# Kernel optimization log

Measured on AMD Instinct MI355X. Metric: run time of the kernel, lower is better.

Reference implementation:

```python
import jax, jax.numpy as jnp
import numpy as np

DIM = 512
H = 8
HS = DIM // H
SCALES = [25, 12, 7]
ATTN_SCALE = HS ** -0.5
EPS = 1e-5


def _ln(x, g, b):
    m = jnp.mean(x, axis=-1, keepdims=True)
    v = jnp.mean((x - m) ** 2, axis=-1, keepdims=True)
    return (x - m) * jax.lax.rsqrt(v + EPS) * g + b


def setup_inputs() -> dict:
    key = jax.random.key(0)
    ks = jax.random.split(key, 12)
    B, T, J, C = 64, 64, 25, DIM
    w = lambda k, s: jax.random.normal(k, s, dtype=jnp.float32) * 0.02
    return {
        "src": jax.random.normal(ks[0], (B, T, J, C), dtype=jnp.float32),
        "spatial_relation": jax.random.normal(ks[1], (B, T, J, J, 2), dtype=jnp.float32),
        "ln1_g": jnp.ones((C,), jnp.float32),
        "ln1_b": jnp.zeros((C,), jnp.float32),
        "Wq": w(ks[2], (3, C, C)),
        "Wk": w(ks[3], (3, C, C)),
        "Wv": w(ks[4], (3, C, C)),
        "pool0_fc1_w": w(ks[5], (C, 2 * C)),
        "pool0_fc1_b": jnp.zeros((2 * C,), jnp.float32),
        "pool0_fc2_w": w(ks[6], (2 * C, SCALES[1])),
        "pool0_fc2_b": jnp.zeros((SCALES[1],), jnp.float32),
        "pool1_fc1_w": w(ks[7], (C, 2 * C)),
        "pool1_fc1_b": jnp.zeros((2 * C,), jnp.float32),
        "pool1_fc2_w": w(ks[8], (2 * C, SCALES[2])),
        "pool1_fc2_b": jnp.zeros((SCALES[2],), jnp.float32),
    }


def reference(src, spatial_relation, ln1_g, ln1_b, Wq, Wk, Wv,
              pool0_fc1_w, pool0_fc1_b, pool0_fc2_w, pool0_fc2_b,
              pool1_fc1_w, pool1_fc1_b, pool1_fc2_w, pool1_fc2_b):
    # NOTE: in the original torch module, the relation-bias terms (R_qk, R_conv,
    # attn_R_qurt) and spatial_relation_emb are computed but never added to the
    # attention logits, so they do not affect the output; faithful output math below.
    B, T, J, C = src.shape
    x = src.reshape(B * T, J, C)
    g_feat = x  # global (query) features, stay at J nodes
    l_feat = x  # local (key/value) features, get pooled
    pools = [
        (pool0_fc1_w, pool0_fc1_b, pool0_fc2_w, pool0_fc2_b),
        (pool1_fc1_w, pool1_fc1_b, pool1_fc2_w, pool1_fc2_b),
    ]
    outs = []
    for i in range(len(SCALES)):
        qn = _ln(g_feat, ln1_g, ln1_b)
        kn = _ln(l_feat, ln1_g, ln1_b)
        q = (qn @ Wq[i]).reshape(B * T, J, H, HS)
        k = (kn @ Wk[i]).reshape(B * T, -1, H, HS)
        v = (kn @ Wv[i]).reshape(B * T, -1, H, HS)
        logits = jnp.einsum('bnhd,bmhd->bhnm', q, k) * ATTN_SCALE
        a = jax.nn.softmax(logits, axis=-1)
        o = jnp.einsum('bhnm,bmhd->bnhd', a, v).reshape(B * T, J, C)
        outs.append(g_feat + o)
        if i < len(SCALES) - 1:
            f1w, f1b, f2w, f2b = pools[i]
            h = jax.nn.gelu(l_feat @ f1w + f1b, approximate=False)
            S = jax.nn.softmax(h @ f2w + f2b, axis=-1)  # (BT, Ni, Ni+1)
            l_feat = jnp.einsum('bns,bnc->bsc', S, l_feat)
    return jnp.mean(jnp.stack(outs, axis=-1), axis=-1)
```

## Files before the change

### kernel.cpp

```cpp
#include <hip/hip_runtime.h>

typedef unsigned short u16;
typedef unsigned int   u32;
typedef _Float16 f16;
typedef __attribute__((ext_vector_type(8))) unsigned short u16x8;
typedef __attribute__((ext_vector_type(8))) _Float16 f16x8;
typedef __attribute__((ext_vector_type(2))) _Float16 f16x2;
typedef __attribute__((ext_vector_type(4))) float f32x4;

__device__ __forceinline__ u16 f2h(float f) {
  f16 h = (f16)f;
  return __builtin_bit_cast(u16, h);
}
__device__ __forceinline__ float h2f(u16 u) {
  return (float)__builtin_bit_cast(f16, u);
}

__global__ __launch_bounds__(256) void prep_w(const float* __restrict__ Wq,
    const float* __restrict__ Wk, const float* __restrict__ Wv,
    const float* __restrict__ f0, const float* __restrict__ f1,
    u16* __restrict__ wt) {
  int t = blockIdx.x * 256 + threadIdx.x;
  float v;
  if (t < 786432) {
    int i = t >> 18, r = t & 262143, n = r >> 9, k = r & 511;
    v = Wq[(size_t)(i << 18) + k * 512 + n];
  } else if (t < 2359296) {
    int r = t - 786432, i = r >> 19, r2 = r & 524287;
    int n = (r2 >> 9) & 511, k = r2 & 511;
    v = ((r2 >> 18) ? Wv : Wk)[(size_t)(i << 18) + k * 512 + n];
  } else if (t < 2883584) {
    int r = t - 2359296, n = r >> 9, k = r & 511;
    v = f0[(size_t)k * 1024 + n];
  } else {
    int r = t - 2883584, n = r >> 9, k = r & 511;
    v = f1[(size_t)k * 1024 + n];
  }
  wt[t] = f2h(v);
}

__global__ __launch_bounds__(256) void ln_f32(const float* __restrict__ x,
    const float* __restrict__ g, const float* __restrict__ bta,
    u16* __restrict__ xn, u16* __restrict__ xb) {
  int row = (blockIdx.x << 2) + (threadIdx.x >> 6);
  int lane = threadIdx.x & 63;
  const float* xr = x + (size_t)row * 512 + (lane << 3);
  float4 a = *(const float4*)xr;
  float4 c = *(const float4*)(xr + 4);
  float v[8] = {a.x, a.y, a.z, a.w, c.x, c.y, c.z, c.w};
  float s = 0.f, s2 = 0.f;
#pragma unroll
  for (int j = 0; j < 8; ++j) { s += v[j]; s2 += v[j] * v[j]; }
  for (int off = 32; off; off >>= 1) { s += __shfl_xor(s, off); s2 += __shfl_xor(s2, off); }
  float mean = s * (1.f / 512.f);
  float var = s2 * (1.f / 512.f) - mean * mean;
  float rs = rsqrtf(var + 1e-5f);
  const float* gp = g + (lane << 3);
  const float* bp = bta + (lane << 3);
  u16x8 pb, pn;
#pragma unroll
  for (int j = 0; j < 8; ++j) {
    pb[j] = f2h(v[j]);
    pn[j] = f2h((v[j] - mean) * rs * gp[j] + bp[j]);
  }
  *(u16x8*)(xb + (size_t)row * 512 + (lane << 3)) = pb;
  *(u16x8*)(xn + (size_t)row * 512 + (lane << 3)) = pn;
}

__global__ __launch_bounds__(256) void ln_b16(const u16* __restrict__ xin,
    const float* __restrict__ g, const float* __restrict__ bta,
    u16* __restrict__ xout) {
  int row = (blockIdx.x << 2) + (threadIdx.x >> 6);
  int lane = threadIdx.x & 63;
  f16x8 u = *(const f16x8*)(xin + (size_t)row * 512 + (lane << 3));
  float v[8];
#pragma unroll
  for (int j = 0; j < 8; ++j) v[j] = (float)u[j];
  float s = 0.f, s2 = 0.f;
#pragma unroll
  for (int j = 0; j < 8; ++j) { s += v[j]; s2 += v[j] * v[j]; }
  for (int off = 32; off; off >>= 1) { s += __shfl_xor(s, off); s2 += __shfl_xor(s2, off); }
  float mean = s * (1.f / 512.f);
  float var = s2 * (1.f / 512.f) - mean * mean;
  float rs = rsqrtf(var + 1e-5f);
  const float* gp = g + (lane << 3);
  const float* bp = bta + (lane << 3);
  u16x8 pn;
#pragma unroll
  for (int j = 0; j < 8; ++j) pn[j] = f2h((v[j] - mean) * rs * gp[j] + bp[j]);
  *(u16x8*)(xout + (size_t)row * 512 + (lane << 3)) = pn;
}

template <bool GELU>
__global__ __launch_bounds__(256, 2) void gemm_bt(const u16* __restrict__ A,
    const u16* __restrict__ Bt, u16* __restrict__ C,
    const float* __restrict__ bias, int M, int N) {
  __shared__ __align__(16) u16 As[128 * 64];
  __shared__ __align__(16) u16 Bs[128 * 64];
  int tid = threadIdx.x;
  int w = tid >> 6, lane = tid & 63;
  int nwg = gridDim.x * gridDim.y;
  int wg = blockIdx.x + gridDim.x * blockIdx.y;
  int swz = (wg & 7) * (nwg >> 3) + (wg >> 3);
  int m0 = (swz / gridDim.x) << 7, n0 = (swz % gridDim.x) << 7;
  int wm = (w & 1) << 6, wn = (w >> 1) << 6;
  f32x4 acc[4][4] = {};
  const int r_off = lane >> 3;
  const int k_off = (lane & 7) << 3;
  for (int kt = 0; kt < 8; ++kt) {
    __syncthreads();
#pragma unroll
    for (int j = 0; j < 4; ++j) {
      int q = (w << 2) + j;
      const u16* gA = A + (size_t)(m0 + (q << 3) + r_off) * 512 + (kt << 6) + k_off;
      __builtin_amdgcn_global_load_lds(
          (const __attribute__((address_space(1))) u32*)gA,
          (__attribute__((address_space(3))) u32*)(As + (q << 9)), 16, 0, 0);
      const u16* gB = Bt + (size_t)(n0 + (q << 3) + r_off) * 512 + (kt << 6) + k_off;
      __builtin_amdgcn_global_load_lds(
          (const __attribute__((address_space(1))) u32*)gB,
          (__attribute__((address_space(3))) u32*)(Bs + (q << 9)), 16, 0, 0);
    }
    asm volatile("s_waitcnt vmcnt(0)" ::: "memory");
    __syncthreads();
#pragma unroll
    for (int kk = 0; kk < 2; ++kk) {
      int ko = (kk << 5) + ((lane >> 4) << 3);
      f16x8 af[4], bfr[4];
#pragma unroll
      for (int mi = 0; mi < 4; ++mi)
        af[mi] = *(const f16x8*)(As + (wm + (mi << 4) + (lane & 15)) * 64 + ko);
#pragma unroll
      for (int ni = 0; ni < 4; ++ni)
        bfr[ni] = *(const f16x8*)(Bs + (wn + (ni << 4) + (lane & 15)) * 64 + ko);
#pragma unroll
      for (int mi = 0; mi < 4; ++mi)
#pragma unroll
        for (int ni = 0; ni < 4; ++ni)
          acc[mi][ni] = __builtin_amdgcn_mfma_f32_16x16x32_f16(af[mi], bfr[ni], acc[mi][ni], 0, 0, 0);
    }
  }
  int cr = (lane >> 4) << 2, cc = lane & 15;
#pragma unroll
  for (int mi = 0; mi < 4; ++mi) {
#pragma unroll
    for (int ni = 0; ni < 4; ++ni) {
      int col = n0 + wn + (ni << 4) + cc;
      float bv = 0.f;
      if (GELU) bv = bias[col];
#pragma unroll
      for (int j = 0; j < 4; ++j) {
        int row = m0 + wm + (mi << 4) + cr + j;
        float v = acc[mi][ni][j];
        if (GELU) { v += bv; v = 0.5f * v * (1.f + erff(v * 0.70710678118f)); }
        C[(size_t)row * N + col] = f2h(v);
      }
    }
  }
}

template <int NKV, int PMODE, int MINW>
__global__ __launch_bounds__(512, MINW) void attn(const u16* __restrict__ Q,
    const u16* __restrict__ KV, const u16* __restrict__ xb,
    float* __restrict__ out, u16* __restrict__ p) {
  constexpr int G = 8;
  constexpr int ELEMS = NKV * 1024;
  __shared__ __align__(16) u16 KVl[2][ELEMS];
  int tid = threadIdx.x;
  int b0 = blockIdx.x * G;
  int h = tid >> 6, r = tid & 63, n = r >> 1, half = r & 1;
  int dbase = (h << 6) + (half << 5);
  {
    const u16* src = KV + (size_t)b0 * ELEMS;
    for (int e = tid * 8; e < ELEMS; e += 4096)
      __builtin_amdgcn_global_load_lds(
          (const __attribute__((address_space(1))) u32*)(src + e),
          (__attribute__((address_space(3))) u32*)(KVl[0] + e), 16, 0, 0);
  }
  asm volatile("s_waitcnt vmcnt(0)" ::: "memory");
  __syncthreads();
  for (int t = 0; t < G; ++t) {
    const u16* KVc = KVl[t & 1];
    if (t + 1 < G) {
      const u16* src = KV + (size_t)(b0 + t + 1) * ELEMS;
      u16* dst = KVl[(t + 1) & 1];
      for (int e = tid * 8; e < ELEMS; e += 4096)
        __builtin_amdgcn_global_load_lds(
            (const __attribute__((address_space(1))) u32*)(src + e),
            (__attribute__((address_space(3))) u32*)(dst + e), 16, 0, 0);
    }
    int b = b0 + t;
    if (n < 25) {
      const u16* qr = Q + (size_t)(b * 25 + n) * 512 + dbase;
      f16x8 q8[4];
#pragma unroll
      for (int i = 0; i < 4; ++i) q8[i] = *(const f16x8*)(qr + (i << 3));
      const f16x2* q2 = (const f16x2*)q8;
      float s[NKV];
      float mx = -1e30f;
#pragma unroll
      for (int m = 0; m < NKV; ++m) {
        const u16* kr = KVc + m * 1024 + dbase;
        f16x2 a0 = {(f16)0.f, (f16)0.f}, a1 = a0;
#pragma unroll
        for (int i = 0; i < 4; ++i) {
          f16x8 kv = *(const f16x8*)(kr + (i << 3));
          const f16x2* k2 = (const f16x2*)&kv;
          a0 += q2[i * 4 + 0] * k2[0];
          a1 += q2[i * 4 + 1] * k2[1];
          a0 += q2[i * 4 + 2] * k2[2];
          a1 += q2[i * 4 + 3] * k2[3];
        }
        f16x2 at = a0 + a1;
        float d = (float)at[0] + (float)at[1];
        d += __shfl_xor(d, 1);
        s[m] = d * 0.125f;
        mx = fmaxf(mx, s[m]);
      }
      float sum = 0.f;
#pragma unroll
      for (int m = 0; m < NKV; ++m) { s[m] = __expf(s[m] - mx); sum += s[m]; }
      f16x8 o8[4] = {};
#pragma unroll
      for (int m = 0; m < NKV; ++m) {
        f16 ah = (f16)s[m];
        f16x8 av = {ah, ah, ah, ah, ah, ah, ah, ah};
        const u16* vr = KVc + m * 1024 + 512 + dbase;
#pragma unroll
        for (int i = 0; i < 4; ++i) {
          f16x8 vv = *(const f16x8*)(vr + (i << 3));
          o8[i] += vv * av;
        }
      }
      size_t rowoff = (size_t)(b * 25 + n) * 512 + dbase;
      if (PMODE == 0 || PMODE == 1) {
        float sc = (1.f / sum) * (1.f / 3.f);
        float* orow = out + rowoff;
        const u16* xrow = xb + rowoff;
#pragma unroll
        for (int i = 0; i < 4; ++i) {
          f16x8 xv;
          if (PMODE == 0) xv = *(const f16x8*)(xrow + (i << 3));
#pragma unroll
          for (int j = 0; j < 8; j += 4) {
            float4 rr;
            if (PMODE == 0) {
              rr.x = (float)o8[i][j + 0] * sc + (float)xv[j + 0];
              rr.y = (float)o8[i][j + 1] * sc + (float)xv[j + 1];
              rr.z = (float)o8[i][j + 2] * sc + (float)xv[j + 2];
              rr.w = (float)o8[i][j + 3] * sc + (float)xv[j + 3];
            } else {
              float4 pv = *(const float4*)(orow + (i << 3) + j);
              rr.x = (float)o8[i][j + 0] * sc + pv.x;
              rr.y = (float)o8[i][j + 1] * sc + pv.y;
              rr.z = (float)o8[i][j + 2] * sc + pv.z;
              rr.w = (float)o8[i][j + 3] * sc + pv.w;
            }
            *(float4*)(orow + (i << 3) + j) = rr;
          }
        }
      } else if (PMODE == 2 || PMODE == 3) {
        float sc = 1.f / sum;
        u16* prow = p + rowoff;
#pragma unroll
        for (int i = 0; i < 4; ++i) {
          u16x8 pk;
          if (PMODE == 3) {
            f16x8 pv = *(const f16x8*)(prow + (i << 3));
#pragma unroll
            for (int j = 0; j < 8; ++j)
              pk[j] = f2h((float)o8[i][j] * sc + (float)pv[j]);
          } else {
#pragma unroll
            for (int j = 0; j < 8; ++j) pk[j] = f2h((float)o8[i][j] * sc);
          }
          *(u16x8*)(prow + (i << 3)) = pk;
        }
      } else {
        float sc = 1.f / sum;
        float* orow = out + rowoff;
        const u16* prow = p + rowoff;
        const u16* xrow = xb + rowoff;
#pragma unroll
        for (int i = 0; i < 4; ++i) {
          f16x8 pv = *(const f16x8*)(prow + (i << 3));
          f16x8 xv = *(const f16x8*)(xrow + (i << 3));
#pragma unroll
          for (int j = 0; j < 8; j += 4) {
            float4 rr;
            rr.x = (float)xv[j + 0] + ((float)pv[j + 0] + (float)o8[i][j + 0] * sc) * (1.f / 3.f);
            rr.y = (float)xv[j + 1] + ((float)pv[j + 1] + (float)o8[i][j + 1] * sc) * (1.f / 3.f);
            rr.z = (float)xv[j + 2] + ((float)pv[j + 2] + (float)o8[i][j + 2] * sc) * (1.f / 3.f);
            rr.w = (float)xv[j + 3] + ((float)pv[j + 3] + (float)o8[i][j + 3] * sc) * (1.f / 3.f);
            *(float4*)(orow + (i << 3) + j) = rr;
          }
        }
      }
    }
    asm volatile("s_waitcnt vmcnt(0)" ::: "memory");
    __syncthreads();
  }
}

template <int NIN, int NOUT>
__global__ __launch_bounds__(256) void pool(const u16* __restrict__ h,
    const u16* __restrict__ lf, const float* __restrict__ w2,
    const float* __restrict__ b2, u16* __restrict__ lout) {
  __shared__ __align__(16) float W2l[1024 * NOUT];
  __shared__ __align__(16) u16 Xl[NIN * 512];
  __shared__ __align__(16) float Sl[NIN * NOUT];
  int b = blockIdx.x, tid = threadIdx.x;
  for (int e = tid; e < 1024 * NOUT; e += 256) W2l[e] = w2[e];
  for (int e = tid * 8; e < NIN * 512; e += 2048)
    *(u16x8*)(Xl + e) = *(const u16x8*)(lf + (size_t)b * NIN * 512 + e);
  __syncthreads();
  if (tid < NIN * 8) {
    int nn = tid >> 3, sub = tid & 7;
    float pl[NOUT] = {};
    const u16* hr = h + (size_t)(b * NIN + nn) * 1024;
    for (int cc = 0; cc < 128; ++cc) {
      int c = sub + (cc << 3);
      float hv = h2f(hr[c]);
#pragma unroll
      for (int s2 = 0; s2 < NOUT; ++s2) pl[s2] += hv * W2l[c * NOUT + s2];
    }
#pragma unroll
    for (int s2 = 0; s2 < NOUT; ++s2) {
      pl[s2] += __shfl_down(pl[s2], 4, 8);
      pl[s2] += __shfl_down(pl[s2], 2, 8);
      pl[s2] += __shfl_down(pl[s2], 1, 8);
    }
    if (sub == 0) {
      float mx = -1e30f;
#pragma unroll
      for (int s2 = 0; s2 < NOUT; ++s2) { pl[s2] += b2[s2]; mx = fmaxf(mx, pl[s2]); }
      float sum = 0.f;
#pragma unroll
      for (int s2 = 0; s2 < NOUT; ++s2) { pl[s2] = __expf(pl[s2] - mx); sum += pl[s2]; }
      float inv = 1.f / sum;
#pragma unroll
      for (int s2 = 0; s2 < NOUT; ++s2) Sl[nn * NOUT + s2] = pl[s2] * inv;
    }
  }
  __syncthreads();
  int c0 = tid << 1;
#pragma unroll
  for (int s2 = 0; s2 < NOUT; ++s2) {
    float a0 = 0.f, a1 = 0.f;
#pragma unroll
    for (int nn = 0; nn < NIN; ++nn) {
      float wv = Sl[nn * NOUT + s2];
      a0 += wv * h2f(Xl[nn * 512 + c0]);
      a1 += wv * h2f(Xl[nn * 512 + c0 + 1]);
    }
    u32 pk = (u32)f2h(a0) | ((u32)f2h(a1) << 16);
    *(u32*)(lout + (size_t)(b * NOUT + s2) * 512 + c0) = pk;
  }
}

extern "C" void kernel_launch(void* const* d_in, const int* in_sizes, int n_in,
                              void* d_out, int out_size, void* d_ws, size_t ws_size,
                              hipStream_t stream) {
  const float* src = (const float*)d_in[0];
  const float* g    = (const float*)d_in[2];
  const float* bt   = (const float*)d_in[3];
  const float* Wq   = (const float*)d_in[4];
  const float* Wk   = (const float*)d_in[5];
  const float* Wv   = (const float*)d_in[6];
  const float* f0w  = (const float*)d_in[7];
  const float* f0b  = (const float*)d_in[8];
  const float* f0w2 = (const float*)d_in[9];
  const float* f0b2 = (const float*)d_in[10];
  const float* f1w  = (const float*)d_in[11];
  const float* f1b  = (const float*)d_in[12];
  const float* f1w2 = (const float*)d_in[13];
  const float* f1b2 = (const float*)d_in[14];
  float* out = (float*)d_out;
  char* ws = (char*)d_ws;

  u16* wt  = (u16*)(ws + 0);
  u16* xn  = (u16*)(ws + 6815744);
  u16* xb  = (u16*)(ws + 111673344);
  u16* qb  = (u16*)(ws + 216530944);
  u16* B1  = (u16*)(ws + 321388544);
  u16* l1  = (u16*)(ws + 426246144);
  u16* kn1 = (u16*)(ws + 476577792);
  u16* l2  = qb;
  u16* kn2 = qb + 14680064;
  bool bigws = ws_size >= 640000000ull;
  u16* pbuf = (u16*)(ws + 526909440);

  prep_w<<<13312, 256, 0, stream>>>(Wq, Wk, Wv, f0w, f1w, wt);
  ln_f32<<<25600, 256, 0, stream>>>(src, g, bt, xn, xb);

  gemm_bt<false><<<dim3(4, 800), 256, 0, stream>>>(xn, wt, qb, nullptr, 102400, 512);
  for (int s = 0; s < 2; ++s) {
    size_t ro = (size_t)s * 51200;
    gemm_bt<false><<<dim3(8, 400), 256, 0, stream>>>(xn + ro * 512, wt + 786432, B1, nullptr, 51200, 1024);
    if (bigws)
      attn<25, 2, 1><<<256, 512, 0, stream>>>(qb + ro * 512, B1, xb + ro * 512, out + ro * 512, pbuf + ro * 512);
    else
      attn<25, 0, 1><<<256, 512, 0, stream>>>(qb + ro * 512, B1, xb + ro * 512, out + ro * 512, pbuf);
  }

  for (int s = 0; s < 2; ++s) {
    size_t ro = (size_t)s * 51200;
    gemm_bt<true><<<dim3(8, 400), 256, 0, stream>>>(xb + ro * 512, wt + 2359296, B1, f0b, 51200, 1024);
    pool<25, 12><<<2048, 256, 0, stream>>>(B1, xb + ro * 512, f0w2, f0b2, l1 + (size_t)s * 2048 * 12 * 512);
  }
  ln_b16<<<12288, 256, 0, stream>>>(l1, g, bt, kn1);

  gemm_bt<false><<<dim3(4, 800), 256, 0, stream>>>(xn, wt + 262144, qb, nullptr, 102400, 512);
  gemm_bt<false><<<dim3(8, 384), 256, 0, stream>>>(kn1, wt + 786432 + 524288, B1, nullptr, 49152, 1024);
  if (bigws)
    attn<12, 3, 2><<<512, 512, 0, stream>>>(qb, B1, xb, out, pbuf);
  else
    attn<12, 1, 2><<<512, 512, 0, stream>>>(qb, B1, xb, out, pbuf);

  gemm_bt<true><<<dim3(8, 384), 256, 0, stream>>>(l1, wt + 2883584, B1, f1b, 49152, 1024);
  pool<12, 7><<<4096, 256, 0, stream>>>(B1, l1, f1w2, f1b2, l2);
  ln_b16<<<7168, 256, 0, stream>>>(l2, g, bt, kn2);

  gemm_bt<false><<<dim3(8, 224), 256, 0, stream>>>(kn2, wt + 786432 + 1048576, B1, nullptr, 28672, 1024);
  gemm_bt<false><<<dim3(4, 800), 256, 0, stream>>>(xn, wt + 524288, qb, nullptr, 102400, 512);
  if (bigws)
    attn<7, 4, 2><<<512, 512, 0, stream>>>(qb, B1, xb, out, pbuf);
  else
    attn<7, 1, 2><<<512, 512, 0, stream>>>(qb, B1, xb, out, pbuf);
}
```

Baseline: 1.569 ms.

## Enlarge GEMM tile to 256x128, stage output via LDS, prefetch attention operands

The GEMM now runs 512 threads per block on a 256x128 output tile, so each loaded B tile is reused across twice as many rows. Results are staged through padded shared memory so they can be written out as coalesced 16-byte rows instead of scattered 2-byte stores. The attention kernel now loads the next Q row and the residual/partial operands before the compute and KV prefetch, to hide global load latency. The cost is higher shared memory use (about 68KB per block), which may lower occupancy, plus more live registers in attention.

```diff
diff --git a/kernel.cpp b/kernel.cpp
--- a/kernel.cpp
+++ b/kernel.cpp
@@ -92,34 +92,39 @@
 }
 
 template <bool GELU>
-__global__ __launch_bounds__(256, 2) void gemm_bt(const u16* __restrict__ A,
+__global__ __launch_bounds__(512, 2) void gemm_bt(const u16* __restrict__ A,
     const u16* __restrict__ Bt, u16* __restrict__ C,
     const float* __restrict__ bias, int M, int N) {
-  __shared__ __align__(16) u16 As[128 * 64];
-  __shared__ __align__(16) u16 Bs[128 * 64];
+  __shared__ __align__(16) char smem[69632];
+  u16* As = (u16*)smem;
+  u16* Bs = (u16*)(smem + 32768);
+  u16* Cs = (u16*)smem;
+  constexpr int LDC = 136;
   int tid = threadIdx.x;
   int w = tid >> 6, lane = tid & 63;
   int nwg = gridDim.x * gridDim.y;
   int wg = blockIdx.x + gridDim.x * blockIdx.y;
   int swz = (wg & 7) * (nwg >> 3) + (wg >> 3);
-  int m0 = (swz / gridDim.x) << 7, n0 = (swz % gridDim.x) << 7;
-  int wm = (w & 1) << 6, wn = (w >> 1) << 6;
+  int m0 = (swz / gridDim.x) << 8, n0 = (swz % gridDim.x) << 7;
+  int wm = (w >> 1) << 6, wn = (w & 1) << 6;
   f32x4 acc[4][4] = {};
-  const int r_off = lane >> 3;
-  const int k_off = (lane & 7) << 3;
+  const int grow = tid >> 3;
+  const int gcol = (tid & 7) << 3;
   for (int kt = 0; kt < 8; ++kt) {
     __syncthreads();
 #pragma unroll
-    for (int j = 0; j < 4; ++j) {
-      int q = (w << 2) + j;
-      const u16* gA = A + (size_t)(m0 + (q << 3) + r_off) * 512 + (kt << 6) + k_off;
+    for (int s = 0; s < 4; ++s) {
+      const u16* gA = A + (size_t)(m0 + grow + (s << 6)) * 512 + (kt << 6) + gcol;
       __builtin_amdgcn_global_load_lds(
           (const __attribute__((address_space(1))) u32*)gA,
-          (__attribute__((address_space(3))) u32*)(As + (q << 9)), 16, 0, 0);
-      const u16* gB = Bt + (size_t)(n0 + (q << 3) + r_off) * 512 + (kt << 6) + k_off;
+          (__attribute__((address_space(3))) u32*)(As + tid * 8 + (s << 12)), 16, 0, 0);
+    }
+#pragma unroll
+    for (int s = 0; s < 2; ++s) {
+      const u16* gB = Bt + (size_t)(n0 + grow + (s << 6)) * 512 + (kt << 6) + gcol;
       __builtin_amdgcn_global_load_lds(
           (const __attribute__((address_space(1))) u32*)gB,
-          (__attribute__((address_space(3))) u32*)(Bs + (q << 9)), 16, 0, 0);
+          (__attribute__((address_space(3))) u32*)(Bs + tid * 8 + (s << 12)), 16, 0, 0);
     }
     asm volatile("s_waitcnt vmcnt(0)" ::: "memory");
     __syncthreads();
@@ -140,23 +145,29 @@
           acc[mi][ni] = __builtin_amdgcn_mfma_f32_16x16x32_f16(af[mi], bfr[ni], acc[mi][ni], 0, 0, 0);
     }
   }
+  __syncthreads();
   int cr = (lane >> 4) << 2, cc = lane & 15;
 #pragma unroll
   for (int mi = 0; mi < 4; ++mi) {
 #pragma unroll
     for (int ni = 0; ni < 4; ++ni) {
-      int col = n0 + wn + (ni << 4) + cc;
       float bv = 0.f;
-      if (GELU) bv = bias[col];
+      if (GELU) bv = bias[n0 + wn + (ni << 4) + cc];
 #pragma unroll
       for (int j = 0; j < 4; ++j) {
-        int row = m0 + wm + (mi << 4) + cr + j;
         float v = acc[mi][ni][j];
         if (GELU) { v += bv; v = 0.5f * v * (1.f + erff(v * 0.70710678118f)); }
-        C[(size_t)row * N + col] = f2h(v);
-      }
-    }
-  }
+        Cs[(wm + (mi << 4) + cr + j) * LDC + wn + (ni << 4) + cc] = f2h(v);
+      }
+    }
+  }
+  __syncthreads();
+  int r = tid >> 1, hc = (tid & 1) << 6;
+  u16* crow = C + (size_t)(m0 + r) * N + n0 + hc;
+  const u16* srow = Cs + r * LDC + hc;
+#pragma unroll
+  for (int i = 0; i < 8; ++i)
+    *(u16x8*)(crow + (i << 3)) = *(const u16x8*)(srow + (i << 3));
 }
 
 template <int NKV, int PMODE, int MINW>
@@ -170,6 +181,14 @@
   int b0 = blockIdx.x * G;
   int h = tid >> 6, r = tid & 63, n = r >> 1, half = r & 1;
   int dbase = (h << 6) + (half << 5);
+  bool act = (n < 25);
+  f16x8 q8[4];
+  if (act) {
+    const u16* qr = Q + (size_t)(b0 * 25 + n) * 512 + dbase;
+#pragma unroll
+    for (int i = 0; i < 4; ++i) q8[i] = *(const f16x8*)(qr + (i << 3));
+  }
+  __builtin_amdgcn_sched_barrier(0);
   {
     const u16* src = KV + (size_t)b0 * ELEMS;
     for (int e = tid * 8; e < ELEMS; e += 4096)
@@ -181,20 +200,44 @@
   __syncthreads();
   for (int t = 0; t < G; ++t) {
     const u16* KVc = KVl[t & 1];
+    int b = b0 + t;
+    size_t rowoff = (size_t)(b * 25 + n) * 512 + dbase;
+    f16x8 pv16[4];
+    f16x8 xv16[4];
+    float4 ov[8];
+    if (act) {
+      if (PMODE == 3 || PMODE == 4) {
+        const u16* prow = p + rowoff;
+#pragma unroll
+        for (int i = 0; i < 4; ++i) pv16[i] = *(const f16x8*)(prow + (i << 3));
+      }
+      if (PMODE == 0 || PMODE == 4) {
+        const u16* xrow = xb + rowoff;
+#pragma unroll
+        for (int i = 0; i < 4; ++i) xv16[i] = *(const f16x8*)(xrow + (i << 3));
+      }
+      if (PMODE == 1) {
+        const float* orow = out + rowoff;
+#pragma unroll
+        for (int i = 0; i < 8; ++i) ov[i] = *(const float4*)(orow + (i << 2));
+      }
+    }
+    f16x8 qn[4];
+    if (act && t + 1 < G) {
+      const u16* qr = Q + (size_t)((b + 1) * 25 + n) * 512 + dbase;
+#pragma unroll
+      for (int i = 0; i < 4; ++i) qn[i] = *(const f16x8*)(qr + (i << 3));
+    }
+    __builtin_amdgcn_sched_barrier(0);
     if (t + 1 < G) {
-      const u16* src = KV + (size_t)(b0 + t + 1) * ELEMS;
+      const u16* src = KV + (size_t)(b + 1) * ELEMS;
       u16* dst = KVl[(t + 1) & 1];
       for (int e = tid * 8; e < ELEMS; e += 4096)
         __builtin_amdgcn_global_load_lds(
             (const __attribute__((address_space(1))) u32*)(src + e),
             (__attribute__((address_space(3))) u32*)(dst + e), 16, 0, 0);
     }
-    int b = b0 + t;
-    if (n < 25) {
-      const u16* qr = Q + (size_t)(b * 25 + n) * 512 + dbase;
-      f16x8 q8[4];
-#pragma unroll
-      for (int i = 0; i < 4; ++i) q8[i] = *(const f16x8*)(qr + (i << 3));
+    if (act) {
       const f16x2* q2 = (const f16x2*)q8;
       float s[NKV];
       float mx = -1e30f;
@@ -232,25 +275,21 @@
           o8[i] += vv * av;
         }
       }
-      size_t rowoff = (size_t)(b * 25 + n) * 512 + dbase;
       if (PMODE == 0 || PMODE == 1) {
         float sc = (1.f / sum) * (1.f / 3.f);
         float* orow = out + rowoff;
-        const u16* xrow = xb + rowoff;
 #pragma unroll
         for (int i = 0; i < 4; ++i) {
-          f16x8 xv;
-          if (PMODE == 0) xv = *(const f16x8*)(xrow + (i << 3));
 #pragma unroll
           for (int j = 0; j < 8; j += 4) {
             float4 rr;
             if (PMODE == 0) {
-              rr.x = (float)o8[i][j + 0] * sc + (float)xv[j + 0];
-              rr.y = (float)o8[i][j + 1] * sc + (float)xv[j + 1];
-              rr.z = (float)o8[i][j + 2] * sc + (float)xv[j + 2];
-              rr.w = (float)o8[i][j + 3] * sc + (float)xv[j + 3];
+              rr.x = (float)o8[i][j + 0] * sc + (float)xv16[i][j + 0];
+              rr.y = (float)o8[i][j + 1] * sc + (float)xv16[i][j + 1];
+              rr.z = (float)o8[i][j + 2] * sc + (float)xv16[i][j + 2];
+              rr.w = (float)o8[i][j + 3] * sc + (float)xv16[i][j + 3];
             } else {
-              float4 pv = *(const float4*)(orow + (i << 3) + j);
+              float4 pv = ov[i * 2 + (j >> 2)];
               rr.x = (float)o8[i][j + 0] * sc + pv.x;
               rr.y = (float)o8[i][j + 1] * sc + pv.y;
               rr.z = (float)o8[i][j + 2] * sc + pv.z;
@@ -265,33 +304,26 @@
 #pragma unroll
         for (int i = 0; i < 4; ++i) {
           u16x8 pk;
-          if (PMODE == 3) {
-            f16x8 pv = *(const f16x8*)(prow + (i << 3));
-#pragma unroll
-            for (int j = 0; j < 8; ++j)
-              pk[j] = f2h((float)o8[i][j] * sc + (float)pv[j]);
-          } else {
-#pragma unroll
-            for (int j = 0; j < 8; ++j) pk[j] = f2h((float)o8[i][j] * sc);
+#pragma unroll
+          for (int j = 0; j < 8; ++j) {
+            float v = (float)o8[i][j] * sc;
+            if (PMODE == 3) v += (float)pv16[i][j];
+            pk[j] = f2h(v);
           }
           *(u16x8*)(prow + (i << 3)) = pk;
         }
       } else {
         float sc = 1.f / sum;
         float* orow = out + rowoff;
-        const u16* prow = p + rowoff;
-        const u16* xrow = xb + rowoff;
 #pragma unroll
         for (int i = 0; i < 4; ++i) {
-          f16x8 pv = *(const f16x8*)(prow + (i << 3));
-          f16x8 xv = *(const f16x8*)(xrow + (i << 3));
 #pragma unroll
           for (int j = 0; j < 8; j += 4) {
             float4 rr;
-            rr.x = (float)xv[j + 0] + ((float)pv[j + 0] + (float)o8[i][j + 0] * sc) * (1.f / 3.f);
-            rr.y = (float)xv[j + 1] + ((float)pv[j + 1] + (float)o8[i][j + 1] * sc) * (1.f / 3.f);
-            rr.z = (float)xv[j + 2] + ((float)pv[j + 2] + (float)o8[i][j + 2] * sc) * (1.f / 3.f);
-            rr.w = (float)xv[j + 3] + ((float)pv[j + 3] + (float)o8[i][j + 3] * sc) * (1.f / 3.f);
+            rr.x = (float)xv16[i][j + 0] + ((float)pv16[i][j + 0] + (float)o8[i][j + 0] * sc) * (1.f / 3.f);
+            rr.y = (float)xv16[i][j + 1] + ((float)pv16[i][j + 1] + (float)o8[i][j + 1] * sc) * (1.f / 3.f);
+            rr.z = (float)xv16[i][j + 2] + ((float)pv16[i][j + 2] + (float)o8[i][j + 2] * sc) * (1.f / 3.f);
+            rr.w = (float)xv16[i][j + 3] + ((float)pv16[i][j + 3] + (float)o8[i][j + 3] * sc) * (1.f / 3.f);
             *(float4*)(orow + (i << 3) + j) = rr;
           }
         }
@@ -299,6 +331,8 @@
     }
     asm volatile("s_waitcnt vmcnt(0)" ::: "memory");
     __syncthreads();
+#pragma unroll
+    for (int i = 0; i < 4; ++i) q8[i] = qn[i];
   }
 }
 
@@ -393,10 +427,10 @@
   prep_w<<<13312, 256, 0, stream>>>(Wq, Wk, Wv, f0w, f1w, wt);
   ln_f32<<<25600, 256, 0, stream>>>(src, g, bt, xn, xb);
 
-  gemm_bt<false><<<dim3(4, 800), 256, 0, stream>>>(xn, wt, qb, nullptr, 102400, 512);
+  gemm_bt<false><<<dim3(4, 400), 512, 0, stream>>>(xn, wt, qb, nullptr, 102400, 512);
   for (int s = 0; s < 2; ++s) {
     size_t ro = (size_t)s * 51200;
-    gemm_bt<false><<<dim3(8, 400), 256, 0, stream>>>(xn + ro * 512, wt + 786432, B1, nullptr, 51200, 1024);
+    gemm_bt<false><<<dim3(8, 200), 512, 0, stream>>>(xn + ro * 512, wt + 786432, B1, nullptr, 51200, 1024);
     if (bigws)
       attn<25, 2, 1><<<256, 512, 0, stream>>>(qb + ro * 512, B1, xb + ro * 512, out + ro * 512, pbuf + ro * 512);
     else
@@ -405,24 +439,24 @@
 
   for (int s = 0; s < 2; ++s) {
     size_t ro = (size_t)s * 51200;
-    gemm_bt<true><<<dim3(8, 400), 256, 0, stream>>>(xb + ro * 512, wt + 2359296, B1, f0b, 51200, 1024);
+    gemm_bt<true><<<dim3(8, 200), 512, 0, stream>>>(xb + ro * 512, wt + 2359296, B1, f0b, 51200, 1024);
     pool<25, 12><<<2048, 256, 0, stream>>>(B1, xb + ro * 512, f0w2, f0b2, l1 + (size_t)s * 2048 * 12 * 512);
   }
   ln_b16<<<12288, 256, 0, stream>>>(l1, g, bt, kn1);
 
-  gemm_bt<false><<<dim3(4, 800), 256, 0, stream>>>(xn, wt + 262144, qb, nullptr, 102400, 512);
-  gemm_bt<false><<<dim3(8, 384), 256, 0, stream>>>(kn1, wt + 786432 + 524288, B1, nullptr, 49152, 1024);
+  gemm_bt<false><<<dim3(4, 400), 512, 0, stream>>>(xn, wt + 262144, qb, nullptr, 102400, 512);
+  gemm_bt<false><<<dim3(8, 192), 512, 0, stream>>>(kn1, wt + 786432 + 524288, B1, nullptr, 49152, 1024);
   if (bigws)
     attn<12, 3, 2><<<512, 512, 0, stream>>>(qb, B1, xb, out, pbuf);
   else
     attn<12, 1, 2><<<512, 512, 0, stream>>>(qb, B1, xb, out, pbuf);
 
-  gemm_bt<true><<<dim3(8, 384), 256, 0, stream>>>(l1, wt + 2883584, B1, f1b, 49152, 1024);
+  gemm_bt<true><<<dim3(8, 192), 512, 0, stream>>>(l1, wt + 2883584, B1, f1b, 49152, 1024);
   pool<12, 7><<<4096, 256, 0, stream>>>(B1, l1, f1w2, f1b2, l2);
   ln_b16<<<7168, 256, 0, stream>>>(l2, g, bt, kn2);
 
-  gemm_bt<false><<<dim3(8, 224), 256, 0, stream>>>(kn2, wt + 786432 + 1048576, B1, nullptr, 28672, 1024);
-  gemm_bt<false><<<dim3(4, 800), 256, 0, stream>>>(xn, wt + 524288, qb, nullptr, 102400, 512);
+  gemm_bt<false><<<dim3(8, 112), 512, 0, stream>>>(kn2, wt + 786432 + 1048576, B1, nullptr, 28672, 1024);
+  gemm_bt<false><<<dim3(4, 400), 512, 0, stream>>>(xn, wt + 524288, qb, nullptr, 102400, 512);
   if (bigws)
     attn<7, 4, 2><<<512, 512, 0, stream>>>(qb, B1, xb, out, pbuf);
   else
```

Result: slower. 2.311 ms (+47.3%).
